# Optimization experiments

Measured on AMD Instinct MI355X. Metric: run time of the kernel, lower is better.

The kernel has to match this reference:

```python
import jax, jax.numpy as jnp
import numpy as np

NEG_SLOPE = 0.2  # PyG GATConv default

def gat_conv(x, src, dst, W, att_src, att_dst, bias, n_nodes):
    """PyG-style GATConv (self-loops already included in src/dst)."""
    H, C = att_src.shape
    h = (x @ W).reshape(n_nodes, H, C)                       # [N,H,C]
    a_src = jnp.einsum('nhc,hc->nh', h, att_src)             # [N,H]
    a_dst = jnp.einsum('nhc,hc->nh', h, att_dst)             # [N,H]
    e = jax.nn.leaky_relu(a_src[src] + a_dst[dst], NEG_SLOPE)  # [E,H]
    # numerically stable segment softmax over incoming edges of each dst node
    e_max = jax.ops.segment_max(e, dst, num_segments=n_nodes)   # [N,H]
    e_exp = jnp.exp(e - e_max[dst])
    denom = jax.ops.segment_sum(e_exp, dst, num_segments=n_nodes)  # [N,H]
    alpha = e_exp / (denom[dst] + 1e-16)                     # [E,H]
    msg = h[src] * alpha[:, :, None]                         # [E,H,C]
    out = jax.ops.segment_sum(msg, dst, num_segments=n_nodes)  # [N,H,C]
    return out.reshape(n_nodes, H * C) + bias

def add_self_loops(edge_index, n_nodes):
    loop = jnp.arange(n_nodes, dtype=edge_index.dtype)
    src = jnp.concatenate([edge_index[0], loop])
    dst = jnp.concatenate([edge_index[1], loop])
    return src, dst

def setup_inputs() -> dict:
    key = jax.random.key(0)
    ks = jax.random.split(key, 12)
    N, E, IN, HID, H1 = 50000, 800000, 128, 64, 4
    s = lambda k, shape, scale: jax.random.normal(k, shape, dtype=jnp.float32) * scale
    return {
        'x': s(ks[0], (N, IN), 1.0),
        'edge_index': jax.random.randint(ks[1], (2, E), 0, N, dtype=jnp.int64),
        'W1': s(ks[2], (IN, H1 * HID), (2.0 / IN) ** 0.5),
        'att_src1': s(ks[3], (H1, HID), 0.1),
        'att_dst1': s(ks[4], (H1, HID), 0.1),
        'b1': s(ks[5], (H1 * HID,), 0.02),
        'W2': s(ks[6], (H1 * HID, HID), (2.0 / (H1 * HID)) ** 0.5),
        'att_src2': s(ks[7], (1, HID), 0.1),
        'att_dst2': s(ks[8], (1, HID), 0.1),
        'b2': s(ks[9], (HID,), 0.02),
        'Ws': s(ks[10], (HID, 1), (2.0 / HID) ** 0.5),
        'bs': s(ks[11], (1,), 0.02),
    }

def reference(x, edge_index, W1, att_src1, att_dst1, b1, W2, att_src2, att_dst2, b2, Ws, bs):
    N = x.shape[0]
    src, dst = add_self_loops(edge_index, N)
    h = jax.nn.elu(gat_conv(x, src, dst, W1, att_src1, att_dst1, b1, N))   # [N,256]
    # dropout is identity in eval mode
    h = jax.nn.elu(gat_conv(h, src, dst, W2, att_src2, att_dst2, b2, N))   # [N,64]
    scores = (h @ Ws + bs).squeeze(-1)                                     # [N]
    return h, scores
```

## Files before the change

kernel.cpp:

```cpp
#include <hip/hip_runtime.h>
#include <hip/hip_bf16.h>
#include <math.h>


#define LRELU_SLOPE 0.2f

typedef __attribute__((ext_vector_type(8))) short short8;
typedef __attribute__((ext_vector_type(4))) float f32x4;

__device__ inline ushort f2bf(float f) {
    uint u = __float_as_uint(f);
    return (ushort)((u + 0x7FFFu + ((u >> 16) & 1u)) >> 16);
}
__device__ inline float bf2f(ushort u) {
    return __uint_as_float(((uint)u) << 16);
}

__device__ inline void prefrag_one(const float* __restrict__ W,
                                   ushort* __restrict__ out,
                                   int tid, int T, int ldn)
{
    int l = tid & 63, jt = tid >> 6;
    int t = jt % T, j = jt / T;
    int n = j * 16 + (l & 15);
    int k0 = t * 32 + (l >> 4) * 8;
    ushort o[8];
    #pragma unroll
    for (int b = 0; b < 8; ++b) o[b] = f2bf(W[(size_t)(k0 + b) * ldn + n]);
    *(short8*)(out + (size_t)tid * 8) = *(short8*)o;
}

__global__ __launch_bounds__(256)
void prep(const float* __restrict__ x, ushort* __restrict__ xbf,
          const float* __restrict__ W1, const float* __restrict__ W2,
          ushort* __restrict__ o1, ushort* __restrict__ o2, int nconv4)
{
    int tid = blockIdx.x * blockDim.x + threadIdx.x;
    if (tid < nconv4) {
        int i = tid << 2;
        float4 v = *(const float4*)(x + i);
        ushort4 o;
        o.x = f2bf(v.x); o.y = f2bf(v.y); o.z = f2bf(v.z); o.w = f2bf(v.w);
        *(ushort4*)(xbf + i) = o;
        return;
    }
    int t = tid - nconv4;
    if (t < 16 * 4 * 64)                 prefrag_one(W1, o1, t, 4, 256);
    else if (t < 16 * 4 * 64 + 4 * 8 * 64)
        prefrag_one(W2, o2, t - 16 * 4 * 64, 8, 64);
}

template<int J, int T, int H>
__global__ __launch_bounds__(256)
void gemm_mfma(const ushort* __restrict__ A, const ushort* __restrict__ Bf,
               ushort* __restrict__ Cbf, const float* __restrict__ attS,
               const float* __restrict__ attD, float* __restrict__ as_,
               float* __restrict__ ad_, int M)
{
    constexpr int K = 32 * T;
    constexpr int NN = 16 * J;
    const int l = threadIdx.x & 63;
    const int wid = blockIdx.x * (blockDim.x >> 6) + (threadIdx.x >> 6);
    const int base = wid * 16;
    if (base >= M) return;
    const int lm = l & 15, lg = l >> 4;

    short8 a[T];
    const ushort* ap = A + (size_t)(base + lm) * K + lg * 8;
    #pragma unroll
    for (int t = 0; t < T; ++t) a[t] = *(const short8*)(ap + t * 32);

    f32x4 acc[J];
    #pragma unroll
    for (int j = 0; j < J; ++j) acc[j] = (f32x4){0.f, 0.f, 0.f, 0.f};

    const ushort* bp = Bf + (size_t)l * 8;
    #pragma unroll
    for (int j = 0; j < J; ++j)
        #pragma unroll
        for (int t = 0; t < T; ++t) {
            short8 b = *(const short8*)(bp + (size_t)(j * T + t) * 512);
            acc[j] = __builtin_amdgcn_mfma_f32_16x16x32_bf16(a[t], b, acc[j], 0, 0, 0);
        }

    float sp[H][4], dp[H][4];
    #pragma unroll
    for (int h = 0; h < H; ++h)
        #pragma unroll
        for (int r = 0; r < 4; ++r) { sp[h][r] = 0.f; dp[h][r] = 0.f; }

    #pragma unroll
    for (int j = 0; j < J; ++j) {
        const int h = j / (J / H);
        const int coff = (j % (J / H)) * 16 + lm;
        float ws = attS[h * 64 + coff];
        float wd = attD[h * 64 + coff];
        #pragma unroll
        for (int r = 0; r < 4; ++r) {
            int row = base + lg * 4 + r;
            Cbf[(size_t)row * NN + j * 16 + lm] = f2bf(acc[j][r]);
            sp[h][r] = fmaf(acc[j][r], ws, sp[h][r]);
            dp[h][r] = fmaf(acc[j][r], wd, dp[h][r]);
        }
    }
    #pragma unroll
    for (int h = 0; h < H; ++h)
        #pragma unroll
        for (int r = 0; r < 4; ++r) {
            float s = sp[h][r], d = dp[h][r];
            s += __shfl_xor(s, 1); d += __shfl_xor(d, 1);
            s += __shfl_xor(s, 2); d += __shfl_xor(d, 2);
            s += __shfl_xor(s, 4); d += __shfl_xor(d, 4);
            s += __shfl_xor(s, 8); d += __shfl_xor(d, 8);
            if (lm == 0) {
                int row = base + lg * 4 + r;
                as_[row * H + h] = s;
                ad_[row * H + h] = d;
            }
        }
}

__global__ __launch_bounds__(256)
void degree_hist(const int* __restrict__ edst, int* __restrict__ deg, int E)
{
    int i = (blockIdx.x * blockDim.x + threadIdx.x) << 2;
    if (i + 3 < E) {
        int4 v = *(const int4*)(edst + i);
        atomicAdd(&deg[v.x], 1); atomicAdd(&deg[v.y], 1);
        atomicAdd(&deg[v.z], 1); atomicAdd(&deg[v.w], 1);
    } else {
        for (; i < E; ++i) atomicAdd(&deg[edst[i]], 1);
    }
}

__global__ __launch_bounds__(1024)
void scan_rowptr(const int* __restrict__ deg, int* __restrict__ rowptr, int N)
{
    __shared__ int wsums[16];
    const int tid = threadIdx.x, lane = tid & 63, wid = tid >> 6;
    const int N4 = N >> 2;
    const int b4 = tid * 13;
    int tsum = 0;
    #pragma unroll
    for (int k = 0; k < 13; ++k) {
        int i4 = b4 + k;
        if (i4 < N4) {
            int4 v = ((const int4*)deg)[i4];
            tsum += (v.x + v.y) + (v.z + v.w);
        }
    }
    int sc = tsum;
    #pragma unroll
    for (int off = 1; off < 64; off <<= 1) {
        int t = __shfl_up(sc, off);
        if (lane >= off) sc += t;
    }
    if (lane == 63) wsums[wid] = sc;
    __syncthreads();
    if (wid == 0) {
        int wv = (lane < 16) ? wsums[lane] : 0;
        #pragma unroll
        for (int off = 1; off < 16; off <<= 1) {
            int t = __shfl_up(wv, off);
            if (lane >= off) wv += t;
        }
        if (lane < 16) wsums[lane] = wv;
    }
    __syncthreads();
    int run = (wid ? wsums[wid - 1] : 0) + sc - tsum;
    #pragma unroll
    for (int k = 0; k < 13; ++k) {
        int i4 = b4 + k;
        if (i4 < N4) {
            int4 v = ((const int4*)deg)[i4];
            int4 o;
            o.x = run; o.y = run + v.x; o.z = o.y + v.y; o.w = o.z + v.z;
            ((int4*)rowptr)[i4] = o;
            run += (v.x + v.y) + (v.z + v.w);
        }
    }
    if (tid == 1023) rowptr[N] = run;
}

__global__ __launch_bounds__(256)
void scatter_edges(const int* __restrict__ esrc, const int* __restrict__ edst,
                   const int* __restrict__ rowptr, int* __restrict__ deg,
                   int* __restrict__ csr_src, int E)
{
    int i = blockIdx.x * blockDim.x + threadIdx.x;
    if (i >= E) return;
    int s = esrc[i], d = edst[i];
    int pos = rowptr[d] + atomicSub(&deg[d], 1) - 1;
    csr_src[pos] = s;
}

__global__ __launch_bounds__(256)
void aggregate_l1(const int* __restrict__ rowptr, const int* __restrict__ csr_src,
                  const ushort* __restrict__ h1, const float* __restrict__ as_,
                  const float* __restrict__ ad_, const float* __restrict__ bias,
                  ushort* __restrict__ outbf, int N)
{
    int w = (blockIdx.x * blockDim.x + threadIdx.x) >> 6;
    int lane = threadIdx.x & 63;
    if (w >= N) return;
    const int head = lane >> 4;
    const int c0 = lane << 2;
    const int my = lane & 3;
    const int hb = lane & 48;
    const float ad = ad_[w * 4 + head];
    float4 acc;
    float dsum;

    {
        float el = as_[w * 4 + head] + ad;
        el = el > 0.f ? el : LRELU_SLOPE * el;
        float p = __expf(el);
        ushort4 u = *(const ushort4*)(h1 + (size_t)w * 256 + c0);
        acc.x = p * bf2f(u.x); acc.y = p * bf2f(u.y);
        acc.z = p * bf2f(u.z); acc.w = p * bf2f(u.w);
        dsum = p;
    }

    int e = rowptr[w];
    const int e1 = rowptr[w + 1];
    for (; e + 3 < e1; e += 4) {
        int s0 = csr_src[e],     s1 = csr_src[e + 1];
        int s2 = csr_src[e + 2], s3 = csr_src[e + 3];
        ushort4 u0 = *(const ushort4*)(h1 + (size_t)s0 * 256 + c0);
        ushort4 u1 = *(const ushort4*)(h1 + (size_t)s1 * 256 + c0);
        ushort4 u2 = *(const ushort4*)(h1 + (size_t)s2 * 256 + c0);
        ushort4 u3 = *(const ushort4*)(h1 + (size_t)s3 * 256 + c0);
        int ms = s0;
        ms = (my == 1) ? s1 : ms;
        ms = (my == 2) ? s2 : ms;
        ms = (my == 3) ? s3 : ms;
        float ev = as_[ms * 4 + head] + ad;
        ev = ev > 0.f ? ev : LRELU_SLOPE * ev;
        float pl = __expf(ev);
        float p0 = __shfl(pl, hb | 0);
        float p1 = __shfl(pl, hb | 1);
        float p2 = __shfl(pl, hb | 2);
        float p3 = __shfl(pl, hb | 3);
        acc.x = fmaf(p0, bf2f(u0.x), acc.x); acc.y = fmaf(p0, bf2f(u0.y), acc.y);
        acc.z = fmaf(p0, bf2f(u0.z), acc.z); acc.w = fmaf(p0, bf2f(u0.w), acc.w);
        acc.x = fmaf(p1, bf2f(u1.x), acc.x); acc.y = fmaf(p1, bf2f(u1.y), acc.y);
        acc.z = fmaf(p1, bf2f(u1.z), acc.z); acc.w = fmaf(p1, bf2f(u1.w), acc.w);
        acc.x = fmaf(p2, bf2f(u2.x), acc.x); acc.y = fmaf(p2, bf2f(u2.y), acc.y);
        acc.z = fmaf(p2, bf2f(u2.z), acc.z); acc.w = fmaf(p2, bf2f(u2.w), acc.w);
        acc.x = fmaf(p3, bf2f(u3.x), acc.x); acc.y = fmaf(p3, bf2f(u3.y), acc.y);
        acc.z = fmaf(p3, bf2f(u3.z), acc.z); acc.w = fmaf(p3, bf2f(u3.w), acc.w);
        dsum += (p0 + p1) + (p2 + p3);
    }
    for (; e < e1; ++e) {
        int s0 = csr_src[e];
        float e0 = as_[s0 * 4 + head] + ad;
        e0 = e0 > 0.f ? e0 : LRELU_SLOPE * e0;
        float p0 = __expf(e0);
        ushort4 u0 = *(const ushort4*)(h1 + (size_t)s0 * 256 + c0);
        acc.x = fmaf(p0, bf2f(u0.x), acc.x); acc.y = fmaf(p0, bf2f(u0.y), acc.y);
        acc.z = fmaf(p0, bf2f(u0.z), acc.z); acc.w = fmaf(p0, bf2f(u0.w), acc.w);
        dsum += p0;
    }
    const float inv = 1.f / (dsum + 1e-16f);
    const float4 b = *(const float4*)(bias + c0);
    float ox = acc.x * inv + b.x; ox = ox > 0.f ? ox : expm1f(ox);
    float oy = acc.y * inv + b.y; oy = oy > 0.f ? oy : expm1f(oy);
    float oz = acc.z * inv + b.z; oz = oz > 0.f ? oz : expm1f(oz);
    float ow = acc.w * inv + b.w; ow = ow > 0.f ? ow : expm1f(ow);
    ushort4 o;
    o.x = f2bf(ox); o.y = f2bf(oy); o.z = f2bf(oz); o.w = f2bf(ow);
    *(ushort4*)(outbf + (size_t)w * 256 + c0) = o;
}

__global__ __launch_bounds__(256)
void aggregate_l2(const int* __restrict__ rowptr, const int* __restrict__ csr_src,
                  const ushort* __restrict__ h2, const float* __restrict__ as_,
                  const float* __restrict__ ad_, const float* __restrict__ b2,
                  const float* __restrict__ Wsv, const float* __restrict__ bs,
                  float* __restrict__ hout, float* __restrict__ scores, int N)
{
    int w = (blockIdx.x * blockDim.x + threadIdx.x) >> 6;
    int lane = threadIdx.x & 63;
    if (w >= N) return;
    const int my = lane & 3;
    const float ad = ad_[w];
    float acc, dsum;
    {
        float el = as_[w] + ad;
        el = el > 0.f ? el : LRELU_SLOPE * el;
        float p = __expf(el);
        acc = p * bf2f(h2[(size_t)w * 64 + lane]);
        dsum = p;
    }
    int e = rowptr[w];
    const int e1 = rowptr[w + 1];
    for (; e + 3 < e1; e += 4) {
        int s0 = csr_src[e],     s1 = csr_src[e + 1];
        int s2 = csr_src[e + 2], s3 = csr_src[e + 3];
        ushort f0 = h2[(size_t)s0 * 64 + lane];
        ushort f1 = h2[(size_t)s1 * 64 + lane];
        ushort f2 = h2[(size_t)s2 * 64 + lane];
        ushort f3 = h2[(size_t)s3 * 64 + lane];
        int ms = s0;
        ms = (my == 1) ? s1 : ms;
        ms = (my == 2) ? s2 : ms;
        ms = (my == 3) ? s3 : ms;
        float ev = as_[ms] + ad;
        ev = ev > 0.f ? ev : LRELU_SLOPE * ev;
        float pl = __expf(ev);
        float p0 = __shfl(pl, 0);
        float p1 = __shfl(pl, 1);
        float p2 = __shfl(pl, 2);
        float p3 = __shfl(pl, 3);
        acc = fmaf(p0, bf2f(f0), acc);
        acc = fmaf(p1, bf2f(f1), acc);
        acc = fmaf(p2, bf2f(f2), acc);
        acc = fmaf(p3, bf2f(f3), acc);
        dsum += (p0 + p1) + (p2 + p3);
    }
    for (; e < e1; ++e) {
        int s0 = csr_src[e];
        float e0 = as_[s0] + ad;
        e0 = e0 > 0.f ? e0 : LRELU_SLOPE * e0;
        float p0 = __expf(e0);
        acc = fmaf(p0, bf2f(h2[(size_t)s0 * 64 + lane]), acc);
        dsum += p0;
    }
    float v = acc / (dsum + 1e-16f) + b2[lane];
    v = v > 0.f ? v : expm1f(v);
    hout[(size_t)w * 64 + lane] = v;
    float sc = v * Wsv[lane];
    #pragma unroll
    for (int off = 32; off; off >>= 1) sc += __shfl_down(sc, off);
    if (lane == 0) scores[w] = sc + bs[0];
}

extern "C" void kernel_launch(void* const* d_in, const int* in_sizes, int n_in,
                              void* d_out, int out_size, void* d_ws, size_t ws_size,
                              hipStream_t stream)
{
    const float* x    = (const float*)d_in[0];
    const int*   ei   = (const int*)d_in[1];
    const float* W1   = (const float*)d_in[2];
    const float* as1w = (const float*)d_in[3];
    const float* ad1w = (const float*)d_in[4];
    const float* b1   = (const float*)d_in[5];
    const float* W2   = (const float*)d_in[6];
    const float* as2w = (const float*)d_in[7];
    const float* ad2w = (const float*)d_in[8];
    const float* b2   = (const float*)d_in[9];
    const float* Ws   = (const float*)d_in[10];
    const float* bs   = (const float*)d_in[11];

    const int N  = in_sizes[0] / 128;
    const int E  = in_sizes[1] / 2;
    const int* esrc = ei;
    const int* edst = ei + E;

    ushort* h1bf  = (ushort*)d_ws;
    ushort* hl1bf = h1bf + (size_t)N * 256;
    ushort* h2bf  = hl1bf + (size_t)N * 256;
    ushort* xbf   = h2bf + (size_t)N * 64;
    ushort* bfr1  = xbf + (size_t)N * 128;
    ushort* bfr2  = bfr1 + 32768;
    float*  as1   = (float*)(bfr2 + 16384);
    float*  ad1   = as1 + (size_t)N * 4;
    float*  as2   = ad1 + (size_t)N * 4;
    float*  ad2   = as2 + N;
    int*    deg    = (int*)(ad2 + N);
    int*    rowptr = deg + N;
    int*    csr_src= rowptr + N + 4;

    float* hout   = (float*)d_out;
    float* scores = hout + (size_t)N * 64;

    hipMemsetAsync(deg, 0, (size_t)N * sizeof(int), stream);
    degree_hist<<<(E / 4 + 255) / 256, 256, 0, stream>>>(edst, deg, E);
    scan_rowptr<<<1, 1024, 0, stream>>>(deg, rowptr, N);
    scatter_edges<<<(E + 255) / 256, 256, 0, stream>>>(
        esrc, edst, rowptr, deg, csr_src, E);

    const int nconv4 = N * 128 / 4;
    prep<<<(nconv4 + 16 * 4 * 64 + 4 * 8 * 64 + 255) / 256, 256, 0, stream>>>(
        x, xbf, W1, W2, bfr1, bfr2, nconv4);

    gemm_mfma<16, 4, 4><<<(N / 16 + 3) / 4, 256, 0, stream>>>(
        xbf, bfr1, h1bf, as1w, ad1w, as1, ad1, N);
    aggregate_l1<<<((size_t)N * 64 + 255) / 256, 256, 0, stream>>>(
        rowptr, csr_src, h1bf, as1, ad1, b1, hl1bf, N);

    gemm_mfma<4, 8, 1><<<(N / 16 + 3) / 4, 256, 0, stream>>>(
        hl1bf, bfr2, h2bf, as2w, ad2w, as2, ad2, N);
    aggregate_l2<<<((size_t)N * 64 + 255) / 256, 256, 0, stream>>>(
        rowptr, csr_src, h2bf, as2, ad2, b2, Ws, bs, hout, scores, N);
}
```

Before: 266.0 us.

## Merge independent front-end kernels into horizontally fused launches

Merges the degree histogram into the bf16 conversion and weight-prefragment kernel, and co-launches the CSR edge scatter with the first MFMA GEMM in a single grid split by block index. Independent work now shares launches and can overlap on the GPU, which cuts the number of kernel launches and the serialized tail of small kernels. The cost is a larger fused grid that mixes heterogeneous blocks with different resource needs, which may hurt occupancy for the GEMM part.

```diff
diff --git a/kernel.cpp b/kernel.cpp
--- a/kernel.cpp
+++ b/kernel.cpp
@@ -31,9 +31,11 @@
 }
 
 __global__ __launch_bounds__(256)
-void prep(const float* __restrict__ x, ushort* __restrict__ xbf,
-          const float* __restrict__ W1, const float* __restrict__ W2,
-          ushort* __restrict__ o1, ushort* __restrict__ o2, int nconv4)
+void fused_front(const float* __restrict__ x, ushort* __restrict__ xbf,
+                 const float* __restrict__ W1, const float* __restrict__ W2,
+                 ushort* __restrict__ o1, ushort* __restrict__ o2,
+                 const int* __restrict__ edst, int* __restrict__ deg,
+                 int nconv4, int E)
 {
     int tid = blockIdx.x * blockDim.x + threadIdx.x;
     if (tid < nconv4) {
@@ -45,22 +47,81 @@
         return;
     }
     int t = tid - nconv4;
-    if (t < 16 * 4 * 64)                 prefrag_one(W1, o1, t, 4, 256);
-    else if (t < 16 * 4 * 64 + 4 * 8 * 64)
-        prefrag_one(W2, o2, t - 16 * 4 * 64, 8, 64);
+    if (t < 16 * 4 * 64) { prefrag_one(W1, o1, t, 4, 256); return; }
+    t -= 16 * 4 * 64;
+    if (t < 4 * 8 * 64)  { prefrag_one(W2, o2, t, 8, 64); return; }
+    t -= 4 * 8 * 64;
+    int i = t << 2;
+    if (i + 3 < E) {
+        int4 v = *(const int4*)(edst + i);
+        atomicAdd(&deg[v.x], 1); atomicAdd(&deg[v.y], 1);
+        atomicAdd(&deg[v.z], 1); atomicAdd(&deg[v.w], 1);
+    } else {
+        for (; i < E; ++i) atomicAdd(&deg[edst[i]], 1);
+    }
+}
+
+__global__ __launch_bounds__(1024)
+void scan_rowptr(const int* __restrict__ deg, int* __restrict__ rowptr, int N)
+{
+    __shared__ int wsums[16];
+    const int tid = threadIdx.x, lane = tid & 63, wid = tid >> 6;
+    const int N4 = N >> 2;
+    const int b4 = tid * 13;
+    int tsum = 0;
+    #pragma unroll
+    for (int k = 0; k < 13; ++k) {
+        int i4 = b4 + k;
+        if (i4 < N4) {
+            int4 v = ((const int4*)deg)[i4];
+            tsum += (v.x + v.y) + (v.z + v.w);
+        }
+    }
+    int sc = tsum;
+    #pragma unroll
+    for (int off = 1; off < 64; off <<= 1) {
+        int t = __shfl_up(sc, off);
+        if (lane >= off) sc += t;
+    }
+    if (lane == 63) wsums[wid] = sc;
+    __syncthreads();
+    if (wid == 0) {
+        int wv = (lane < 16) ? wsums[lane] : 0;
+        #pragma unroll
+        for (int off = 1; off < 16; off <<= 1) {
+            int t = __shfl_up(wv, off);
+            if (lane >= off) wv += t;
+        }
+        if (lane < 16) wsums[lane] = wv;
+    }
+    __syncthreads();
+    int run = (wid ? wsums[wid - 1] : 0) + sc - tsum;
+    #pragma unroll
+    for (int k = 0; k < 13; ++k) {
+        int i4 = b4 + k;
+        if (i4 < N4) {
+            int4 v = ((const int4*)deg)[i4];
+            int4 o;
+            o.x = run; o.y = run + v.x; o.z = o.y + v.y; o.w = o.z + v.z;
+            ((int4*)rowptr)[i4] = o;
+            run += (v.x + v.y) + (v.z + v.w);
+        }
+    }
+    if (tid == 1023) rowptr[N] = run;
 }
 
 template<int J, int T, int H>
-__global__ __launch_bounds__(256)
-void gemm_mfma(const ushort* __restrict__ A, const ushort* __restrict__ Bf,
-               ushort* __restrict__ Cbf, const float* __restrict__ attS,
-               const float* __restrict__ attD, float* __restrict__ as_,
-               float* __restrict__ ad_, int M)
+__device__ inline void gemm_body(int wid, const ushort* __restrict__ A,
+                                 const ushort* __restrict__ Bf,
+                                 ushort* __restrict__ Cbf,
+                                 const float* __restrict__ attS,
+                                 const float* __restrict__ attD,
+                                 float* __restrict__ as_,
+                                 float* __restrict__ ad_, int M)
 {
     constexpr int K = 32 * T;
     constexpr int NN = 16 * J;
     const int l = threadIdx.x & 63;
-    const int wid = blockIdx.x * (blockDim.x >> 6) + (threadIdx.x >> 6);
     const int base = wid * 16;
     if (base >= M) return;
     const int lm = l & 15, lg = l >> 4;
@@ -121,77 +182,35 @@
 }
 
 __global__ __launch_bounds__(256)
-void degree_hist(const int* __restrict__ edst, int* __restrict__ deg, int E)
-{
-    int i = (blockIdx.x * blockDim.x + threadIdx.x) << 2;
-    if (i + 3 < E) {
-        int4 v = *(const int4*)(edst + i);
-        atomicAdd(&deg[v.x], 1); atomicAdd(&deg[v.y], 1);
-        atomicAdd(&deg[v.z], 1); atomicAdd(&deg[v.w], 1);
-    } else {
-        for (; i < E; ++i) atomicAdd(&deg[edst[i]], 1);
-    }
-}
-
-__global__ __launch_bounds__(1024)
-void scan_rowptr(const int* __restrict__ deg, int* __restrict__ rowptr, int N)
-{
-    __shared__ int wsums[16];
-    const int tid = threadIdx.x, lane = tid & 63, wid = tid >> 6;
-    const int N4 = N >> 2;
-    const int b4 = tid * 13;
-    int tsum = 0;
-    #pragma unroll
-    for (int k = 0; k < 13; ++k) {
-        int i4 = b4 + k;
-        if (i4 < N4) {
-            int4 v = ((const int4*)deg)[i4];
-            tsum += (v.x + v.y) + (v.z + v.w);
-        }
-    }
-    int sc = tsum;
-    #pragma unroll
-    for (int off = 1; off < 64; off <<= 1) {
-        int t = __shfl_up(sc, off);
-        if (lane >= off) sc += t;
-    }
-    if (lane == 63) wsums[wid] = sc;
-    __syncthreads();
-    if (wid == 0) {
-        int wv = (lane < 16) ? wsums[lane] : 0;
-        #pragma unroll
-        for (int off = 1; off < 16; off <<= 1) {
-            int t = __shfl_up(wv, off);
-            if (lane >= off) wv += t;
-        }
-        if (lane < 16) wsums[lane] = wv;
-    }
-    __syncthreads();
-    int run = (wid ? wsums[wid - 1] : 0) + sc - tsum;
-    #pragma unroll
-    for (int k = 0; k < 13; ++k) {
-        int i4 = b4 + k;
-        if (i4 < N4) {
-            int4 v = ((const int4*)deg)[i4];
-            int4 o;
-            o.x = run; o.y = run + v.x; o.z = o.y + v.y; o.w = o.z + v.z;
-            ((int4*)rowptr)[i4] = o;
-            run += (v.x + v.y) + (v.z + v.w);
-        }
-    }
-    if (tid == 1023) rowptr[N] = run;
-}
-
-__global__ __launch_bounds__(256)
-void scatter_edges(const int* __restrict__ esrc, const int* __restrict__ edst,
+void scatter_gemm1(const ushort* __restrict__ A, const ushort* __restrict__ Bf,
+                   ushort* __restrict__ Cbf, const float* __restrict__ attS,
+                   const float* __restrict__ attD, float* __restrict__ as_,
+                   float* __restrict__ ad_, int M, int gemmBlocks,
+                   const int* __restrict__ esrc, const int* __restrict__ edst,
                    const int* __restrict__ rowptr, int* __restrict__ deg,
                    int* __restrict__ csr_src, int E)
 {
-    int i = blockIdx.x * blockDim.x + threadIdx.x;
+    if ((int)blockIdx.x < gemmBlocks) {
+        int wid = blockIdx.x * (blockDim.x >> 6) + (threadIdx.x >> 6);
+        gemm_body<16, 4, 4>(wid, A, Bf, Cbf, attS, attD, as_, ad_, M);
+        return;
+    }
+    int i = (blockIdx.x - gemmBlocks) * blockDim.x + threadIdx.x;
     if (i >= E) return;
     int s = esrc[i], d = edst[i];
     int pos = rowptr[d] + atomicSub(&deg[d], 1) - 1;
     csr_src[pos] = s;
+}
+
+template<int J, int T, int H>
+__global__ __launch_bounds__(256)
+void gemm_mfma(const ushort* __restrict__ A, const ushort* __restrict__ Bf,
+               ushort* __restrict__ Cbf, const float* __restrict__ attS,
+               const float* __restrict__ attD, float* __restrict__ as_,
+               float* __restrict__ ad_, int M)
+{
+    int wid = blockIdx.x * (blockDim.x >> 6) + (threadIdx.x >> 6);
+    gemm_body<J, T, H>(wid, A, Bf, Cbf, attS, attD, as_, ad_, M);
 }
 
 __global__ __launch_bounds__(256)
@@ -375,22 +394,27 @@
     float* scores = hout + (size_t)N * 64;
 
     hipMemsetAsync(deg, 0, (size_t)N * sizeof(int), stream);
-    degree_hist<<<(E / 4 + 255) / 256, 256, 0, stream>>>(edst, deg, E);
+
+    const int nconv4 = N * 128 / 4;
+    const int nfrag  = 16 * 4 * 64 + 4 * 8 * 64;
+    const int nhist  = (E + 3) / 4;
+    fused_front<<<(nconv4 + nfrag + nhist + 255) / 256, 256, 0, stream>>>(
+        x, xbf, W1, W2, bfr1, bfr2, edst, deg, nconv4, E);
+
     scan_rowptr<<<1, 1024, 0, stream>>>(deg, rowptr, N);
-    scatter_edges<<<(E + 255) / 256, 256, 0, stream>>>(
+
+    const int gemmBlocks    = (N / 16 + 3) / 4;
+    const int scatterBlocks = (E + 255) / 256;
+    scatter_gemm1<<<gemmBlocks + scatterBlocks, 256, 0, stream>>>(
+        xbf, bfr1, h1bf, as1w, ad1w, as1, ad1, N, gemmBlocks,
         esrc, edst, rowptr, deg, csr_src, E);
 
-    const int nconv4 = N * 128 / 4;
-    prep<<<(nconv4 + 16 * 4 * 64 + 4 * 8 * 64 + 255) / 256, 256, 0, stream>>>(
-        x, xbf, W1, W2, bfr1, bfr2, nconv4);
-
-    gemm_mfma<16, 4, 4><<<(N / 16 + 3) / 4, 256, 0, stream>>>(
-        xbf, bfr1, h1bf, as1w, ad1w, as1, ad1, N);
     aggregate_l1<<<((size_t)N * 64 + 255) / 256, 256, 0, stream>>>(
         rowptr, csr_src, h1bf, as1, ad1, b1, hl1bf, N);
 
     gemm_mfma<4, 8, 1><<<(N / 16 + 3) / 4, 256, 0, stream>>>(
         hl1bf, bfr2, h2bf, as2w, ad2w, as2, ad2, N);
+
     aggregate_l2<<<((size_t)N * 64 + 255) / 256, 256, 0, stream>>>(
         rowptr, csr_src, h2bf, as2, ad2, b2, Ws, bs, hout, scores, N);
 }
```

After: 249.5 us. 1.07x faster.
